# Performance work log

Hardware: AMD Instinct MI355X
Metric: run time of the kernel (lower is better)

Reference implementation:

```python
import jax, jax.numpy as jnp
import numpy as np

B, S, H = 2, 2048, 2048
NH, NKV, D = 32, 8, 64
GROUPS = NH // NKV
SCALE = D ** -0.5


def rotate_half(x):
    x1, x2 = x[..., : D // 2], x[..., D // 2 :]
    return jnp.concatenate((-x2, x1), axis=-1)


def setup_inputs() -> dict:
    key = jax.random.key(0)
    ks = jax.random.split(key, 8)
    x = jax.random.normal(ks[0], (B, S, H), dtype=jnp.float32)
    cos = jax.random.uniform(ks[1], (B, S, D), dtype=jnp.float32)
    sin = jax.random.uniform(ks[2], (B, S, D), dtype=jnp.float32)
    mask = jnp.tril(jnp.ones((S, S), dtype=jnp.int32))[None, None]  # causal (1,1,S,S)
    std = H ** -0.5
    wq = jax.random.normal(ks[3], (NH * D, H), dtype=jnp.float32) * std
    wk = jax.random.normal(ks[4], (NKV * D, H), dtype=jnp.float32) * std
    wv = jax.random.normal(ks[5], (NKV * D, H), dtype=jnp.float32) * std
    wo = jax.random.normal(ks[6], (H, NH * D), dtype=jnp.float32) * std
    return {"x": x, "cos": cos, "sin": sin, "mask": mask,
            "wq": wq, "wk": wk, "wv": wv, "wo": wo}


def reference(x, cos, sin, mask, wq, wk, wv, wo):
    b, s, _ = x.shape
    # projections (Linear: x @ W^T, no bias)
    q = (x @ wq.T).reshape(b, s, NH, D).transpose(0, 2, 1, 3)    # (b, nh, s, d)
    k = (x @ wk.T).reshape(b, s, NKV, D).transpose(0, 2, 1, 3)   # (b, nkv, s, d)
    v = (x @ wv.T).reshape(b, s, NKV, D).transpose(0, 2, 1, 3)
    # RoPE
    c = cos[:, None, :, :]
    sn = sin[:, None, :, :]
    q = q * c + rotate_half(q) * sn
    k = k * c + rotate_half(k) * sn
    # GQA: repeat KV heads
    k = jnp.repeat(k, GROUPS, axis=1)   # (b, nh, s, d)
    v = jnp.repeat(v, GROUPS, axis=1)
    scores = jnp.einsum("bhqd,bhkd->bhqk", q, k) * SCALE
    scores = jnp.where(mask == 0, -jnp.inf, scores)
    weights = jax.nn.softmax(scores, axis=-1)
    out = jnp.einsum("bhqk,bhkd->bhqd", weights, v)
    out = out.transpose(0, 2, 1, 3).reshape(b, s, NH * D)
    return out @ wo.T
```

## Files before the change

kernel.cpp:

```cpp
#include <hip/hip_runtime.h>
#include <hip/hip_bf16.h>
#include <math.h>

typedef __attribute__((ext_vector_type(8))) short bf16x8;
typedef __attribute__((ext_vector_type(4))) float f32x4;

__device__ __forceinline__ float bf2f(ushort u) {
  union { unsigned u; float f; } v; v.u = ((unsigned)u) << 16; return v.f;
}
__device__ __forceinline__ ushort f2bf(float f) {
  union { float f; unsigned u; } v; v.f = f;
  unsigned r = v.u + 0x7FFFu + ((v.u >> 16) & 1u);
  return (ushort)(r >> 16);
}
#if __has_builtin(__builtin_amdgcn_exp2f)
#define EXP2F(x) __builtin_amdgcn_exp2f(x)
#else
#define EXP2F(x) exp2f(x)
#endif
__device__ __forceinline__ void gl_lds16(const ushort* g, ushort* l) {
  __builtin_amdgcn_global_load_lds(
      (const __attribute__((address_space(1))) unsigned int*)g,
      (__attribute__((address_space(3))) unsigned int*)l, 16, 0, 0);
}

static const long XB   = 0;
static const long WQB  = 8388608;
static const long WKB  = 12582912;
static const long WVB  = 13631488;
static const long WOB  = 14680064;
static const long COSB = 18874368;
static const long SINB = 19136512;
static const long QB   = 19398656;
static const long KB   = 27787264;
static const long VTB  = 29884416;

__global__ void detect_dtype(const ushort* __restrict__ x, int* __restrict__ flag) {
  __shared__ int cnt;
  if (threadIdx.x == 0) cnt = 0;
  __syncthreads();
  int local = 0;
  for (int j = 0; j < 32; j++) {
    ushort u = x[threadIdx.x + j * 256];
    int e = (u >> 7) & 0xFF;
    if (e >= 100 && e <= 142) local++;
  }
  atomicAdd(&cnt, local);
  __syncthreads();
  if (threadIdx.x == 0) *flag = (cnt >= 6554) ? 1 : 0;
}

__global__ void cast_all(const void* __restrict__ s0, const void* __restrict__ s1,
                         const void* __restrict__ s2, const void* __restrict__ s3,
                         const void* __restrict__ s4, const void* __restrict__ s5,
                         const void* __restrict__ s6,
                         ushort* __restrict__ d0, ushort* __restrict__ d1,
                         ushort* __restrict__ d2, ushort* __restrict__ d3,
                         ushort* __restrict__ d4, ushort* __restrict__ d5,
                         ushort* __restrict__ d6, const int* __restrict__ flag) {
  if (*flag) return;
  const long N = 2424832;
  for (long i = (long)blockIdx.x * blockDim.x + threadIdx.x; i < N;
       i += (long)gridDim.x * blockDim.x) {
    const float4* s; ushort* d; long off;
    if      (i < 1048576) { s = (const float4*)s0; d = d0; off = i; }
    else if (i < 1572864) { s = (const float4*)s1; d = d1; off = i - 1048576; }
    else if (i < 1703936) { s = (const float4*)s2; d = d2; off = i - 1572864; }
    else if (i < 1835008) { s = (const float4*)s3; d = d3; off = i - 1703936; }
    else if (i < 2359296) { s = (const float4*)s4; d = d4; off = i - 1835008; }
    else if (i < 2392064) { s = (const float4*)s5; d = d5; off = i - 2359296; }
    else                  { s = (const float4*)s6; d = d6; off = i - 2392064; }
    float4 a = s[2 * off], b = s[2 * off + 1];
    uint4 o;
    o.x = (unsigned)f2bf(a.x) | ((unsigned)f2bf(a.y) << 16);
    o.y = (unsigned)f2bf(a.z) | ((unsigned)f2bf(a.w) << 16);
    o.z = (unsigned)f2bf(b.x) | ((unsigned)f2bf(b.y) << 16);
    o.w = (unsigned)f2bf(b.z) | ((unsigned)f2bf(b.w) << 16);
    ((uint4*)d)[off] = o;
  }
}

__device__ __forceinline__ void gemm_body(
    const ushort* __restrict__ A, const ushort* __restrict__ W, void* __restrict__ C,
    int N, int K, int bm, int bn, bool ofp32, ushort* As, ushort* Ws) {
  const int tid = threadIdx.x;
  const int wave = tid >> 6, lane = tid & 63;
  const int quad = lane >> 4, l15 = lane & 15;
  const int wm = (wave >> 1) * 64, wn = (wave & 1) * 64;
  const int srow = tid >> 2, sk = (tid & 3) * 8;
  const ushort* Ap = A + (size_t)(bm + srow) * K + sk;
  const ushort* Wp = W + (size_t)(bn + srow) * K + sk;
  ushort* AsW = As + wave * 512;
  ushort* WsW = Ws + wave * 512;
  f32x4 acc[4][4] = {};
  for (int k0 = 0; k0 < K; k0 += 32) {
    __syncthreads();
    gl_lds16(Ap + k0, AsW);
    gl_lds16(Ap + (size_t)64 * K + k0, AsW + 2048);
    gl_lds16(Wp + k0, WsW);
    gl_lds16(Wp + (size_t)64 * K + k0, WsW + 2048);
    __syncthreads();
    bf16x8 af[4], wf[4];
#pragma unroll
    for (int t = 0; t < 4; t++)
      af[t] = *(const bf16x8*)&As[(wm + t * 16 + l15) * 32 + quad * 8];
#pragma unroll
    for (int t = 0; t < 4; t++)
      wf[t] = *(const bf16x8*)&Ws[(wn + t * 16 + l15) * 32 + quad * 8];
#pragma unroll
    for (int mt = 0; mt < 4; mt++)
#pragma unroll
      for (int nt = 0; nt < 4; nt++)
        acc[mt][nt] = __builtin_amdgcn_mfma_f32_16x16x32_bf16(af[mt], wf[nt], acc[mt][nt], 0, 0, 0);
  }
  if (!ofp32) {
    ushort* Cb = (ushort*)C;
#pragma unroll
    for (int mt = 0; mt < 4; mt++)
#pragma unroll
      for (int nt = 0; nt < 4; nt++)
#pragma unroll
        for (int r = 0; r < 4; r++) {
          int row = bm + wm + mt * 16 + quad * 4 + r;
          int col = bn + wn + nt * 16 + l15;
          Cb[(size_t)row * N + col] = f2bf(acc[mt][nt][r]);
        }
  } else {
    float* Cf = (float*)C;
#pragma unroll
    for (int mt = 0; mt < 4; mt++)
#pragma unroll
      for (int nt = 0; nt < 4; nt++)
#pragma unroll
        for (int r = 0; r < 4; r++) {
          int row = bm + wm + mt * 16 + quad * 4 + r;
          int col = bn + wn + nt * 16 + l15;
          Cf[(size_t)row * N + col] = acc[mt][nt][r];
        }
  }
}

__global__ __launch_bounds__(256) void gemm_qkv(
    const ushort* __restrict__ xws, const ushort* __restrict__ xorig,
    const ushort* __restrict__ wqws, const ushort* __restrict__ wqorig,
    const ushort* __restrict__ wkws, const ushort* __restrict__ wkorig,
    const ushort* __restrict__ wvws, const ushort* __restrict__ wvorig,
    ushort* __restrict__ qout, ushort* __restrict__ kout, ushort* __restrict__ vtout,
    const int* __restrict__ flag) {
  __shared__ __align__(16) ushort As[128 * 32];
  __shared__ __align__(16) ushort Ws[128 * 32];
  const bool bf = (*flag != 0);
  const ushort* x = bf ? xorig : xws;
  const int id = blockIdx.x;
  if (id < 512) {
    gemm_body(x, bf ? wqorig : wqws, qout, 2048, 2048, (id >> 4) * 128, (id & 15) * 128, false, As, Ws);
  } else if (id < 640) {
    int t = id - 512;
    gemm_body(x, bf ? wkorig : wkws, kout, 512, 2048, (t >> 2) * 128, (t & 3) * 128, false, As, Ws);
  } else {
    int t = id - 640;
    gemm_body(bf ? wvorig : wvws, x, vtout, 4096, 2048, (t & 3) * 128, (t >> 2) * 128, false, As, Ws);
  }
}

__global__ __launch_bounds__(256) void gemm_bt(
    const ushort* __restrict__ Aws, const ushort* __restrict__ Aorig,
    const ushort* __restrict__ Wws, const ushort* __restrict__ Worig,
    void* __restrict__ C, int N, int K, const int* __restrict__ flag, int outMode) {
  __shared__ __align__(16) ushort As[128 * 32];
  __shared__ __align__(16) ushort Ws[128 * 32];
  const bool bf = (*flag != 0);
  const ushort* A = (bf && Aorig) ? Aorig : Aws;
  const ushort* W = (bf && Worig) ? Worig : Wws;
  bool ofp32 = (outMode == 1) && !bf;
  gemm_body(A, W, C, N, K, blockIdx.y * 128, blockIdx.x * 128, ofp32, As, Ws);
}

__global__ void rope_kernel(ushort* __restrict__ Kb,
                            const ushort* __restrict__ cws, const ushort* __restrict__ corig,
                            const ushort* __restrict__ sws, const ushort* __restrict__ sorig,
                            const int* __restrict__ flag) {
  const ushort* cb = (*flag) ? corig : cws;
  const ushort* sb = (*flag) ? sorig : sws;
  int j = blockIdx.x * 256 + threadIdx.x;
  long row = j >> 5; int rest = j & 31; int c8 = (rest & 3) * 8;
  ushort* base = Kb + row * 512 + (rest >> 2) * 64 + c8;
  uint4 lo4 = *(const uint4*)base;
  uint4 hi4 = *(const uint4*)(base + 32);
  uint4 cl4 = *(const uint4*)(cb + row * 64 + c8);
  uint4 ch4 = *(const uint4*)(cb + row * 64 + c8 + 32);
  uint4 sl4 = *(const uint4*)(sb + row * 64 + c8);
  uint4 sh4 = *(const uint4*)(sb + row * 64 + c8 + 32);
  const ushort* lo = (const ushort*)&lo4; const ushort* hi = (const ushort*)&hi4;
  const ushort* cl = (const ushort*)&cl4; const ushort* ch = (const ushort*)&ch4;
  const ushort* sl = (const ushort*)&sl4; const ushort* sh = (const ushort*)&sh4;
  uint4 olo, ohi;
  ushort* po = (ushort*)&olo; ushort* ph = (ushort*)&ohi;
#pragma unroll
  for (int k = 0; k < 8; k++) {
    float l = bf2f(lo[k]), h = bf2f(hi[k]);
    po[k] = f2bf(l * bf2f(cl[k]) - h * bf2f(sl[k]));
    ph[k] = f2bf(h * bf2f(ch[k]) + l * bf2f(sh[k]));
  }
  *(uint4*)base = olo;
  *(uint4*)(base + 32) = ohi;
}

__global__ __launch_bounds__(512, 4) void attn_kernel(
    const ushort* __restrict__ Qb, const ushort* __restrict__ Kb,
    const ushort* __restrict__ Vt,
    const ushort* __restrict__ cws, const ushort* __restrict__ corig,
    const ushort* __restrict__ sws, const ushort* __restrict__ sorig,
    ushort* __restrict__ Ob, const int* __restrict__ flag) {
  __shared__ __align__(16) ushort Ks[2][4096];
  __shared__ __align__(16) ushort Vs[2][4096];
  __shared__ __align__(16) ushort Ps[128 * 72];
  const int tid = threadIdx.x;
  const int wave = tid >> 6, lane = tid & 63;
  const int quad = lane >> 4, l15 = lane & 15;
  const int id = blockIdx.x;
  const int kvh = id & 7;
  const int b = (id >> 3) & 1;
  const int hsub = (id >> 4) & 3;
  const int h = kvh * 4 + hsub;
  const int t = 15 - (id >> 6);
  const size_t brow = (size_t)b * 2048;
  const ushort* Kg = Kb + brow * 512 + (size_t)kvh * 64;
  const ushort* Vg = Vt + (size_t)(kvh * 64) * 4096 + brow;

  const int prow = wave * 16 + (lane >> 2);
  const int chunk = (lane & 3) * 8;
  const int k_s = prow & 63, k_kc = prow >> 6;
  const int v_d = prow & 63, v_sc = prow >> 6;
  const int ldsW = wave * 512;

  const int q0 = t * 128;
  const int wrow0 = q0 + wave * 16;
  const int blockNt = 2 * t + 2;
  const int myLast = wrow0 >> 6;

  gl_lds16(Kg + (size_t)k_s * 512 + k_kc * 32 + chunk, &Ks[0][ldsW]);
  gl_lds16(Vg + (size_t)v_d * 4096 + v_sc * 32 + chunk, &Vs[0][ldsW]);

  const ushort* cb = (*flag) ? corig : cws;
  const ushort* sp = (*flag) ? sorig : sws;
  const size_t qrow_g = brow + wrow0 + l15;
  bf16x8 qlo = *(const bf16x8*)&Qb[qrow_g * 2048 + h * 64 + quad * 8];
  bf16x8 qhi = *(const bf16x8*)&Qb[qrow_g * 2048 + h * 64 + 32 + quad * 8];
  bf16x8 cl = *(const bf16x8*)&cb[qrow_g * 64 + quad * 8];
  bf16x8 ch = *(const bf16x8*)&cb[qrow_g * 64 + 32 + quad * 8];
  bf16x8 sl = *(const bf16x8*)&sp[qrow_g * 64 + quad * 8];
  bf16x8 sh = *(const bf16x8*)&sp[qrow_g * 64 + 32 + quad * 8];
  bf16x8 qf[2];
  const float scl = 0.18033688011112f;
#pragma unroll
  for (int j = 0; j < 8; j++) {
    float l = bf2f((ushort)qlo[j]), hg = bf2f((ushort)qhi[j]);
    qf[0][j] = (short)f2bf((l * bf2f((ushort)cl[j]) - hg * bf2f((ushort)sl[j])) * scl);
    qf[1][j] = (short)f2bf((hg * bf2f((ushort)ch[j]) + l * bf2f((ushort)sh[j])) * scl);
  }

  float l_loc = 0.f;
  f32x4 oacc[4] = {};

  __syncthreads();

  for (int nt = 0; nt < blockNt; nt++) {
    const int cur = nt & 1;
    if (nt + 1 < blockNt) {
      const int n1 = (nt + 1) * 64;
      gl_lds16(Kg + (size_t)(n1 + k_s) * 512 + k_kc * 32 + chunk, &Ks[cur ^ 1][ldsW]);
      gl_lds16(Vg + (size_t)v_d * 4096 + n1 + v_sc * 32 + chunk, &Vs[cur ^ 1][ldsW]);
    }
    if (nt <= myLast) {
      const int n0 = nt * 64;
      const ushort* Kc = Ks[cur];
      const ushort* Vc = Vs[cur];
      f32x4 sc[4];
      __builtin_amdgcn_s_setprio(1);
#pragma unroll
      for (int ct = 0; ct < 4; ct++) {
        bf16x8 kf0 = *(const bf16x8*)&Kc[(ct * 16 + l15) * 32 + quad * 8];
        bf16x8 kf1 = *(const bf16x8*)&Kc[2048 + (ct * 16 + l15) * 32 + quad * 8];
        f32x4 z = {0.f, 0.f, 0.f, 0.f};
        z = __builtin_amdgcn_mfma_f32_16x16x32_bf16(kf0, qf[0], z, 0, 0, 0);
        z = __builtin_amdgcn_mfma_f32_16x16x32_bf16(kf1, qf[1], z, 0, 0, 0);
        sc[ct] = z;
      }
      __builtin_amdgcn_s_setprio(0);
      if (nt == myLast) {
        const int qrow = wrow0 + l15;
#pragma unroll
        for (int ct = 0; ct < 4; ct++)
#pragma unroll
          for (int r = 0; r < 4; r++)
            if (n0 + ct * 16 + quad * 4 + r > qrow) sc[ct][r] = -INFINITY;
      }
#pragma unroll
      for (int ct = 0; ct < 4; ct++)
#pragma unroll
        for (int k = 0; k < 2; k++) {
          float pv0 = EXP2F(sc[ct][2 * k]     - 23.083120654223f);
          float pv1 = EXP2F(sc[ct][2 * k + 1] - 23.083120654223f);
          l_loc += pv0 + pv1;
          unsigned u = ((__float_as_uint(pv0) + 0x8000u) >> 16) |
                       ((__float_as_uint(pv1) + 0x8000u) & 0xFFFF0000u);
          *(unsigned*)&Ps[(wave * 16 + l15) * 72 + ct * 16 + quad * 4 + 2 * k] = u;
        }
      bf16x8 pf0 = *(const bf16x8*)&Ps[(wave * 16 + l15) * 72 + quad * 8];
      bf16x8 pf1 = *(const bf16x8*)&Ps[(wave * 16 + l15) * 72 + 32 + quad * 8];
      __builtin_amdgcn_s_setprio(1);
#pragma unroll
      for (int dt = 0; dt < 4; dt++) {
        bf16x8 vf0 = *(const bf16x8*)&Vc[(dt * 16 + l15) * 32 + quad * 8];
        bf16x8 vf1 = *(const bf16x8*)&Vc[2048 + (dt * 16 + l15) * 32 + quad * 8];
        oacc[dt] = __builtin_amdgcn_mfma_f32_16x16x32_bf16(pf0, vf0, oacc[dt], 0, 0, 0);
        oacc[dt] = __builtin_amdgcn_mfma_f32_16x16x32_bf16(pf1, vf1, oacc[dt], 0, 0, 0);
      }
      __builtin_amdgcn_s_setprio(0);
    }
    __syncthreads();
  }
  l_loc += __shfl_xor(l_loc, 16, 64);
  l_loc += __shfl_xor(l_loc, 32, 64);
  float linv[4];
#pragma unroll
  for (int r = 0; r < 4; r++) linv[r] = 1.f / __shfl(l_loc, quad * 4 + r, 64);
#pragma unroll
  for (int dt = 0; dt < 4; dt++)
#pragma unroll
    for (int r = 0; r < 4; r++) {
      int s = wrow0 + quad * 4 + r;
      Ob[(brow + s) * 2048 + h * 64 + dt * 16 + l15] = f2bf(oacc[dt][r] * linv[r]);
    }
}

extern "C" void kernel_launch(void* const* d_in, const int* in_sizes, int n_in,
                              void* d_out, int out_size, void* d_ws, size_t ws_size,
                              hipStream_t stream) {
  char* wsb = (char*)d_ws;
  int* flag = (int*)wsb;
  ushort* base = (ushort*)(wsb + 256);
  ushort* xb   = base + XB;
  ushort* wqb  = base + WQB;
  ushort* wkb  = base + WKB;
  ushort* wvb  = base + WVB;
  ushort* wob  = base + WOB;
  ushort* cosb = base + COSB;
  ushort* sinb = base + SINB;
  ushort* qb   = base + QB;
  ushort* kb   = base + KB;
  ushort* vtb  = base + VTB;
  ushort* abuf = xb;

  const ushort* xo  = (const ushort*)d_in[0];
  const ushort* co  = (const ushort*)d_in[1];
  const ushort* so  = (const ushort*)d_in[2];
  const ushort* wqo = (const ushort*)d_in[4];
  const ushort* wko = (const ushort*)d_in[5];
  const ushort* wvo = (const ushort*)d_in[6];
  const ushort* woo = (const ushort*)d_in[7];

  detect_dtype<<<1, 256, 0, stream>>>(xo, flag);

  cast_all<<<4096, 256, 0, stream>>>(d_in[0], d_in[4], d_in[5], d_in[6], d_in[7],
                                     d_in[1], d_in[2],
                                     xb, wqb, wkb, wvb, wob, cosb, sinb, flag);

  gemm_qkv<<<768, 256, 0, stream>>>(xb, xo, wqb, wqo, wkb, wko, wvb, wvo,
                                    qb, kb, vtb, flag);

  rope_kernel<<<512, 256, 0, stream>>>(kb, cosb, co, sinb, so, flag);

  attn_kernel<<<1024, 512, 0, stream>>>(qb, kb, vtb, cosb, co, sinb, so, abuf, flag);

  gemm_bt<<<dim3(16, 32), 256, 0, stream>>>(abuf, nullptr, wob, woo, d_out, 2048, 2048, flag, 1);
}
```

Before: 314.0 us.

## Fold dtype detection into cast kernel, double GEMM K-step, split softmax sums

Dtype detection now runs redundantly inside every cast_all block, so the separate single-block launch is gone. The GEMM body loads a 64-wide K slab per barrier pair instead of 32, halving the synchronisations and doubling LDS per block. The attention inner loop keeps two partial row sums for more ILP and uses the HIP bf16x2 packing intrinsic with round-to-nearest-even instead of manual rounding. Costs are redundant detection reads in all 4096 cast blocks and possibly lower GEMM occupancy from the larger LDS footprint.

```diff
diff --git a/kernel.cpp b/kernel.cpp
--- a/kernel.cpp
+++ b/kernel.cpp
@@ -35,21 +35,6 @@
 static const long KB   = 27787264;
 static const long VTB  = 29884416;
 
-__global__ void detect_dtype(const ushort* __restrict__ x, int* __restrict__ flag) {
-  __shared__ int cnt;
-  if (threadIdx.x == 0) cnt = 0;
-  __syncthreads();
-  int local = 0;
-  for (int j = 0; j < 32; j++) {
-    ushort u = x[threadIdx.x + j * 256];
-    int e = (u >> 7) & 0xFF;
-    if (e >= 100 && e <= 142) local++;
-  }
-  atomicAdd(&cnt, local);
-  __syncthreads();
-  if (threadIdx.x == 0) *flag = (cnt >= 6554) ? 1 : 0;
-}
-
 __global__ void cast_all(const void* __restrict__ s0, const void* __restrict__ s1,
                          const void* __restrict__ s2, const void* __restrict__ s3,
                          const void* __restrict__ s4, const void* __restrict__ s5,
@@ -57,8 +42,22 @@
                          ushort* __restrict__ d0, ushort* __restrict__ d1,
                          ushort* __restrict__ d2, ushort* __restrict__ d3,
                          ushort* __restrict__ d4, ushort* __restrict__ d5,
-                         ushort* __restrict__ d6, const int* __restrict__ flag) {
-  if (*flag) return;
+                         ushort* __restrict__ d6, int* __restrict__ flag) {
+  __shared__ int cnt;
+  if (threadIdx.x == 0) cnt = 0;
+  __syncthreads();
+  const ushort* xu = (const ushort*)s0;
+  int local = 0;
+  for (int j = 0; j < 32; j++) {
+    ushort u = xu[threadIdx.x + j * 256];
+    int e = (u >> 7) & 0xFF;
+    if (e >= 100 && e <= 142) local++;
+  }
+  atomicAdd(&cnt, local);
+  __syncthreads();
+  const bool isbf = (cnt >= 6554);
+  if (threadIdx.x == 0 && blockIdx.x == 0) *flag = isbf ? 1 : 0;
+  if (isbf) return;
   const long N = 2424832;
   for (long i = (long)blockIdx.x * blockDim.x + threadIdx.x; i < N;
        i += (long)gridDim.x * blockDim.x) {
@@ -93,25 +92,34 @@
   ushort* AsW = As + wave * 512;
   ushort* WsW = Ws + wave * 512;
   f32x4 acc[4][4] = {};
-  for (int k0 = 0; k0 < K; k0 += 32) {
+  for (int k0 = 0; k0 < K; k0 += 64) {
     __syncthreads();
     gl_lds16(Ap + k0, AsW);
     gl_lds16(Ap + (size_t)64 * K + k0, AsW + 2048);
+    gl_lds16(Ap + k0 + 32, AsW + 4096);
+    gl_lds16(Ap + (size_t)64 * K + k0 + 32, AsW + 6144);
     gl_lds16(Wp + k0, WsW);
     gl_lds16(Wp + (size_t)64 * K + k0, WsW + 2048);
+    gl_lds16(Wp + k0 + 32, WsW + 4096);
+    gl_lds16(Wp + (size_t)64 * K + k0 + 32, WsW + 6144);
     __syncthreads();
-    bf16x8 af[4], wf[4];
-#pragma unroll
-    for (int t = 0; t < 4; t++)
-      af[t] = *(const bf16x8*)&As[(wm + t * 16 + l15) * 32 + quad * 8];
-#pragma unroll
-    for (int t = 0; t < 4; t++)
-      wf[t] = *(const bf16x8*)&Ws[(wn + t * 16 + l15) * 32 + quad * 8];
-#pragma unroll
-    for (int mt = 0; mt < 4; mt++)
-#pragma unroll
-      for (int nt = 0; nt < 4; nt++)
-        acc[mt][nt] = __builtin_amdgcn_mfma_f32_16x16x32_bf16(af[mt], wf[nt], acc[mt][nt], 0, 0, 0);
+#pragma unroll
+    for (int p = 0; p < 2; p++) {
+      const ushort* AsB = As + p * 4096;
+      const ushort* WsB = Ws + p * 4096;
+      bf16x8 af[4], wf[4];
+#pragma unroll
+      for (int t = 0; t < 4; t++)
+        af[t] = *(const bf16x8*)&AsB[(wm + t * 16 + l15) * 32 + quad * 8];
+#pragma unroll
+      for (int t = 0; t < 4; t++)
+        wf[t] = *(const bf16x8*)&WsB[(wn + t * 16 + l15) * 32 + quad * 8];
+#pragma unroll
+      for (int mt = 0; mt < 4; mt++)
+#pragma unroll
+        for (int nt = 0; nt < 4; nt++)
+          acc[mt][nt] = __builtin_amdgcn_mfma_f32_16x16x32_bf16(af[mt], wf[nt], acc[mt][nt], 0, 0, 0);
+    }
   }
   if (!ofp32) {
     ushort* Cb = (ushort*)C;
@@ -147,8 +155,8 @@
     const ushort* __restrict__ wvws, const ushort* __restrict__ wvorig,
     ushort* __restrict__ qout, ushort* __restrict__ kout, ushort* __restrict__ vtout,
     const int* __restrict__ flag) {
-  __shared__ __align__(16) ushort As[128 * 32];
-  __shared__ __align__(16) ushort Ws[128 * 32];
+  __shared__ __align__(16) ushort As[2 * 4096];
+  __shared__ __align__(16) ushort Ws[2 * 4096];
   const bool bf = (*flag != 0);
   const ushort* x = bf ? xorig : xws;
   const int id = blockIdx.x;
@@ -167,8 +175,8 @@
     const ushort* __restrict__ Aws, const ushort* __restrict__ Aorig,
     const ushort* __restrict__ Wws, const ushort* __restrict__ Worig,
     void* __restrict__ C, int N, int K, const int* __restrict__ flag, int outMode) {
-  __shared__ __align__(16) ushort As[128 * 32];
-  __shared__ __align__(16) ushort Ws[128 * 32];
+  __shared__ __align__(16) ushort As[2 * 4096];
+  __shared__ __align__(16) ushort Ws[2 * 4096];
   const bool bf = (*flag != 0);
   const ushort* A = (bf && Aorig) ? Aorig : Aws;
   const ushort* W = (bf && Worig) ? Worig : Wws;
@@ -260,7 +268,7 @@
     qf[1][j] = (short)f2bf((hg * bf2f((ushort)ch[j]) + l * bf2f((ushort)sh[j])) * scl);
   }
 
-  float l_loc = 0.f;
+  float lsum0 = 0.f, lsum1 = 0.f;
   f32x4 oacc[4] = {};
 
   __syncthreads();
@@ -302,10 +310,10 @@
         for (int k = 0; k < 2; k++) {
           float pv0 = EXP2F(sc[ct][2 * k]     - 23.083120654223f);
           float pv1 = EXP2F(sc[ct][2 * k + 1] - 23.083120654223f);
-          l_loc += pv0 + pv1;
-          unsigned u = ((__float_as_uint(pv0) + 0x8000u) >> 16) |
-                       ((__float_as_uint(pv1) + 0x8000u) & 0xFFFF0000u);
-          *(unsigned*)&Ps[(wave * 16 + l15) * 72 + ct * 16 + quad * 4 + 2 * k] = u;
+          lsum0 += pv0;
+          lsum1 += pv1;
+          __hip_bfloat162 pk = __float22bfloat162_rn(make_float2(pv0, pv1));
+          *(__hip_bfloat162*)&Ps[(wave * 16 + l15) * 72 + ct * 16 + quad * 4 + 2 * k] = pk;
         }
       bf16x8 pf0 = *(const bf16x8*)&Ps[(wave * 16 + l15) * 72 + quad * 8];
       bf16x8 pf1 = *(const bf16x8*)&Ps[(wave * 16 + l15) * 72 + 32 + quad * 8];
@@ -321,6 +329,7 @@
     }
     __syncthreads();
   }
+  float l_loc = lsum0 + lsum1;
   l_loc += __shfl_xor(l_loc, 16, 64);
   l_loc += __shfl_xor(l_loc, 32, 64);
   float linv[4];
@@ -361,8 +370,6 @@
   const ushort* wvo = (const ushort*)d_in[6];
   const ushort* woo = (const ushort*)d_in[7];
 
-  detect_dtype<<<1, 256, 0, stream>>>(xo, flag);
-
   cast_all<<<4096, 256, 0, stream>>>(d_in[0], d_in[4], d_in[5], d_in[6], d_in[7],
                                      d_in[1], d_in[2],
                                      xb, wqb, wkb, wvb, wob, cosb, sinb, flag);
```

Measured after the change: 318.9 us. Within noise of the previous version (+1.6%).
